# Kernel tuning notes

Measured on AMD Instinct MI355X. Metric: run time of the kernel, lower is better.

The kernel has to match this reference:

```python
import jax, jax.numpy as jnp
import numpy as np

N, E = 50000, 800000
IN, HID, HEADS, EDIM, OUT = 128, 32, 4, 16, 1
W = HID * HEADS  # 128, encoder width


def _glorot(key, shape):
    fan_in = shape[0]
    return jax.random.normal(key, shape, dtype=jnp.float32) / np.sqrt(fan_in)


def setup_inputs() -> dict:
    key = jax.random.key(0)
    ks = jax.random.split(key, 24)
    inp = {
        "x": jax.random.normal(ks[0], (N, IN), dtype=jnp.float32),
        "edge_index": jax.random.randint(ks[1], (2, E), 0, N, dtype=jnp.int64),
        "edge_attr": jax.random.normal(ks[2], (E, EDIM), dtype=jnp.float32),
        # layer 0 (in_channels -> heads*hidden)
        "Wl0": _glorot(ks[3], (IN, W)), "bl0": jnp.zeros((W,), jnp.float32),
        "Wr0": _glorot(ks[4], (IN, W)), "br0": jnp.zeros((W,), jnp.float32),
        "We0": _glorot(ks[5], (EDIM, W)),
        "att0": _glorot(ks[6], (HEADS, HID)),
        "b0": jnp.zeros((W,), jnp.float32),
        # layer 1 (heads*hidden -> heads*hidden)
        "Wl1": _glorot(ks[7], (W, W)), "bl1": jnp.zeros((W,), jnp.float32),
        "Wr1": _glorot(ks[8], (W, W)), "br1": jnp.zeros((W,), jnp.float32),
        "We1": _glorot(ks[9], (EDIM, W)),
        "att1": _glorot(ks[10], (HEADS, HID)),
        "b1": jnp.zeros((W,), jnp.float32),
        # classifier
        "Wc": _glorot(ks[11], (W, OUT)), "bc": jnp.zeros((OUT,), jnp.float32),
    }
    return inp


def _gatv2_layer(x, src, dst, ea, Wl, bl, Wr, br, We, att, b, n_nodes):
    # GATv2Conv (PyG defaults: share_weights=False, negative_slope=0.2, concat=True)
    H, C = att.shape
    xl = (x @ Wl + bl).reshape(n_nodes, H, C)   # source-side transform
    xr = (x @ Wr + br).reshape(n_nodes, H, C)   # target-side transform
    eh = (ea @ We).reshape(-1, H, C)            # edge feature transform (no bias)
    m = xl[src] + xr[dst] + eh                  # [E', H, C] per-edge message pre-activation
    e = jnp.einsum('ehc,hc->eh', jax.nn.leaky_relu(m, 0.2), att)  # [E', H]
    # segment softmax over incoming edges of each dst node (self-loops ensure no empty segment)
    emax = jax.ops.segment_max(e, dst, num_segments=n_nodes)
    ex = jnp.exp(e - emax[dst])
    denom = jax.ops.segment_sum(ex, dst, num_segments=n_nodes)
    alpha = ex / (denom[dst] + 1e-16)
    out = jax.ops.segment_sum(alpha[..., None] * xl[src], dst, num_segments=n_nodes)
    return out.reshape(n_nodes, H * C) + b


def reference(x, edge_index, edge_attr,
              Wl0, bl0, Wr0, br0, We0, att0, b0,
              Wl1, bl1, Wr1, br1, We1, att1, b1,
              Wc, bc):
    n = x.shape[0]
    src, dst = edge_index[0], edge_index[1]
    # add_self_loops with fill_value='mean': self-loop edge_attr = mean of incoming edge_attr per node
    cnt = jax.ops.segment_sum(jnp.ones((src.shape[0],), x.dtype), dst, num_segments=n)
    loop_attr = jax.ops.segment_sum(edge_attr, dst, num_segments=n) / jnp.maximum(cnt, 1.0)[:, None]
    loop = jnp.arange(n, dtype=src.dtype)
    src_a = jnp.concatenate([src, loop])
    dst_a = jnp.concatenate([dst, loop])
    ea_a = jnp.concatenate([edge_attr, loop_attr], axis=0)

    h = jax.nn.gelu(_gatv2_layer(x, src_a, dst_a, ea_a, Wl0, bl0, Wr0, br0, We0, att0, b0, n), approximate=False)
    h = jax.nn.gelu(_gatv2_layer(h, src_a, dst_a, ea_a, Wl1, bl1, Wr1, br1, We1, att1, b1, n), approximate=False)
    logits = h @ Wc + bc  # [N, 1]  (dropout inactive in eval mode)
    return logits.squeeze(-1)
```

## Files before the change

kernel.cpp:

```cpp
#include <hip/hip_runtime.h>
#include <math.h>


static inline size_t align256(size_t x) { return (x + 255) & ~size_t(255); }

__device__ __forceinline__ int clampi(int v, int lo, int hi) {
  return v < lo ? lo : (v > hi ? hi : v);
}

__global__ void k_loop_accum(const int* __restrict__ ei, const float* __restrict__ ea,
                             float* __restrict__ lsum, int* __restrict__ cnt, int E, int n) {
  int i = blockIdx.x * blockDim.x + threadIdx.x;
  if (i >= E * 16) return;
  int e = i >> 4, d = i & 15;
  int dst = clampi(ei[E + e], 0, n - 1);
  atomicAdd(&lsum[dst * 16 + d], ea[i]);
  if (d == 0) atomicAdd(&cnt[dst], 1);
}

__global__ void k_loop_final(float* __restrict__ lsum, const int* __restrict__ cnt, int n) {
  int i = blockIdx.x * blockDim.x + threadIdx.x;
  if (i >= n * 16) return;
  int node = i >> 4;
  int c = cnt[node];
  lsum[i] = lsum[i] / (float)(c > 1 ? c : 1);
}

__global__ void k_scan(const int* __restrict__ cnt, int* __restrict__ row_ptr, int n) {
  const int T = 512;
  __shared__ int wsum[8], wbase[8];
  int tid = threadIdx.x;
  int chunk = (n + T - 1) / T;
  int lo = tid * chunk; if (lo > n) lo = n;
  int hi = lo + chunk;  if (hi > n) hi = n;
  int s = 0;
  for (int i = lo; i < hi; ++i) s += cnt[i] + 1;
  int lane = tid & 63, w = tid >> 6;
  int incl = s;
  #pragma unroll
  for (int d = 1; d < 64; d <<= 1) {
    int v = __shfl_up(incl, d, 64);
    if (lane >= d) incl += v;
  }
  if (lane == 63) wsum[w] = incl;
  __syncthreads();
  if (tid == 0) {
    int a = 0;
    for (int i = 0; i < 8; ++i) { wbase[i] = a; a += wsum[i]; }
  }
  __syncthreads();
  int run = wbase[w] + (incl - s);
  if (tid == 0) row_ptr[0] = 0;
  for (int i = lo; i < hi; ++i) { run += cnt[i] + 1; row_ptr[i + 1] = run; }
}

__global__ void k_scatter(const int* __restrict__ ei, int* __restrict__ cursor,
                          int* __restrict__ col_src, int* __restrict__ col_eid, int E, int n) {
  int i = blockIdx.x * blockDim.x + threadIdx.x;
  if (i < E) {
    int src = clampi(ei[i], 0, n - 1);
    int dst = clampi(ei[E + i], 0, n - 1);
    int pos = atomicAdd(&cursor[dst], 1);
    col_src[pos] = src;
    col_eid[pos] = i;
  } else if (i < E + n) {
    int node = i - E;
    int pos = atomicAdd(&cursor[node], 1);
    col_src[pos] = node;
    col_eid[pos] = E + node;
  }
}

__launch_bounds__(256)
__global__ void k_transform(const float* __restrict__ in, const float* __restrict__ Wl,
                            const float* __restrict__ bl, const float* __restrict__ Wr,
                            const float* __restrict__ br, float* __restrict__ xl,
                            float* __restrict__ xr, int n) {
  __shared__ float As[16][128];
  int tid = threadIdx.x;
  int row0 = blockIdx.x * 16;
  int rows = n - row0; if (rows > 16) rows = 16;
  const float4* in4 = (const float4*)(in + (size_t)row0 * 128);
  float4* As4 = (float4*)As;
  for (int i = tid; i < rows * 32; i += 256) As4[i] = in4[i];
  __syncthreads();
  int c = tid;
  const float* B = (c < 128) ? Wl : Wr;
  int cc = c & 127;
  float bias = (c < 128) ? bl[cc] : br[cc];
  float acc[16];
  #pragma unroll
  for (int i = 0; i < 16; ++i) acc[i] = bias;
  for (int k = 0; k < 128; k += 4) {
    float b0 = B[(k + 0) * 128 + cc], b1 = B[(k + 1) * 128 + cc];
    float b2 = B[(k + 2) * 128 + cc], b3 = B[(k + 3) * 128 + cc];
    #pragma unroll
    for (int r = 0; r < 16; ++r) {
      float4 a = *(const float4*)&As[r][k];
      acc[r] += a.x * b0 + a.y * b1 + a.z * b2 + a.w * b3;
    }
  }
  float* op = (c < 128) ? xl : xr;
  for (int r = 0; r < rows; ++r) op[(size_t)(row0 + r) * 128 + cc] = acc[r];
}

__launch_bounds__(256)
__global__ void k_aggregate(const float* __restrict__ xl, const float* __restrict__ xr,
                            const int* __restrict__ row_ptr, const int* __restrict__ col_src,
                            const int* __restrict__ col_eid, const float* __restrict__ ea,
                            const float* __restrict__ loop_attr, const float* __restrict__ We,
                            const float* __restrict__ att, const float* __restrict__ bvec,
                            float* __restrict__ out, int n, int E) {
  int wv = threadIdx.x >> 6, lane = threadIdx.x & 63;
  int node = blockIdx.x * 4 + wv;
  if (node >= n) return;
  int c0 = lane * 2, c1 = lane * 2 + 1;
  float we0[16], we1[16];
  #pragma unroll
  for (int d = 0; d < 16; ++d) {
    we0[d] = We[d * 128 + c0];
    we1[d] = We[d * 128 + c1];
  }
  float att0 = att[c0], att1 = att[c1];
  float2 xrv = ((const float2*)(xr + (size_t)node * 128))[lane];
  float mx = -INFINITY, den = 0.f, acc0 = 0.f, acc1 = 0.f;
  int beg = row_ptr[node], end = row_ptr[node + 1];
  #pragma unroll 4
  for (int i = beg; i < end; ++i) {
    int src = col_src[i];
    int eid = col_eid[i];
    const float4* eap = (eid < E) ? (const float4*)(ea + (size_t)eid * 16)
                                  : (const float4*)(loop_attr + (size_t)(eid - E) * 16);
    float2 xlv = ((const float2*)(xl + (size_t)src * 128))[lane];
    float eh0 = 0.f, eh1 = 0.f;
    #pragma unroll
    for (int q = 0; q < 4; ++q) {
      float4 v = eap[q];
      eh0 += v.x * we0[q * 4 + 0] + v.y * we0[q * 4 + 1] + v.z * we0[q * 4 + 2] + v.w * we0[q * 4 + 3];
      eh1 += v.x * we1[q * 4 + 0] + v.y * we1[q * 4 + 1] + v.z * we1[q * 4 + 2] + v.w * we1[q * 4 + 3];
    }
    float m0 = xlv.x + xrv.x + eh0;
    float m1 = xlv.y + xrv.y + eh1;
    float l0 = m0 > 0.f ? m0 : 0.2f * m0;
    float l1 = m1 > 0.f ? m1 : 0.2f * m1;
    float p = l0 * att0 + l1 * att1;
    p += __shfl_xor(p, 1);
    p += __shfl_xor(p, 2);
    p += __shfl_xor(p, 4);
    p += __shfl_xor(p, 8);
    float nm = fmaxf(mx, p);
    float sc = expf(mx - nm);
    float w  = expf(p - nm);
    den  = den  * sc + w;
    acc0 = acc0 * sc + w * xlv.x;
    acc1 = acc1 * sc + w * xlv.y;
    mx = nm;
  }
  float inv = 1.f / (den + 1e-16f);
  float2 bv = ((const float2*)bvec)[lane];
  float o0 = acc0 * inv + bv.x;
  float o1 = acc1 * inv + bv.y;
  o0 = 0.5f * o0 * (1.f + erff(o0 * 0.70710678118654752f));
  o1 = 0.5f * o1 * (1.f + erff(o1 * 0.70710678118654752f));
  ((float2*)(out + (size_t)node * 128))[lane] = make_float2(o0, o1);
}

__global__ void k_classifier(const float* __restrict__ h, const float* __restrict__ Wc,
                             const float* __restrict__ bc, float* __restrict__ out, int n) {
  int node = blockIdx.x * blockDim.x + threadIdx.x;
  if (node >= n) return;
  const float4* hp = (const float4*)(h + (size_t)node * 128);
  const float4* wp = (const float4*)Wc;
  float acc = 0.f;
  #pragma unroll
  for (int k = 0; k < 32; ++k) {
    float4 a = hp[k];
    float4 w = wp[k];
    acc += a.x * w.x + a.y * w.y + a.z * w.z + a.w * w.w;
  }
  out[node] = acc + bc[0];
}

extern "C" void kernel_launch(void* const* d_in, const int* in_sizes, int n_in,
                              void* d_out, int out_size, void* d_ws, size_t ws_size,
                              hipStream_t stream) {
  const float* x    = (const float*)d_in[0];
  const int*   ei   = (const int*)d_in[1];
  const float* ea   = (const float*)d_in[2];
  const float* Wl0  = (const float*)d_in[3];
  const float* bl0  = (const float*)d_in[4];
  const float* Wr0  = (const float*)d_in[5];
  const float* br0  = (const float*)d_in[6];
  const float* We0  = (const float*)d_in[7];
  const float* att0 = (const float*)d_in[8];
  const float* b0   = (const float*)d_in[9];
  const float* Wl1  = (const float*)d_in[10];
  const float* bl1  = (const float*)d_in[11];
  const float* Wr1  = (const float*)d_in[12];
  const float* br1  = (const float*)d_in[13];
  const float* We1  = (const float*)d_in[14];
  const float* att1 = (const float*)d_in[15];
  const float* b1   = (const float*)d_in[16];
  const float* Wc   = (const float*)d_in[17];
  const float* bc   = (const float*)d_in[18];
  float* out = (float*)d_out;

  int n  = in_sizes[0] / 128;
  int E  = in_sizes[1] / 2;
  int Ep = E + n;

  char* ws = (char*)d_ws;
  size_t off = 0;
  auto alloc = [&](size_t bytes) { size_t o = off; off = align256(off + bytes); return o; };
  int*   cnt     = (int*)  (ws + alloc((size_t)n * 4));
  float* lsum    = (float*)(ws + alloc((size_t)n * 16 * 4));
  int*   row_ptr = (int*)  (ws + alloc((size_t)(n + 1) * 4));
  int*   cursor  = (int*)  (ws + alloc((size_t)n * 4));
  int*   col_src = (int*)  (ws + alloc((size_t)Ep * 4));
  int*   col_eid = (int*)  (ws + alloc((size_t)Ep * 4));
  float* xl      = (float*)(ws + alloc((size_t)n * 128 * 4));
  float* xr      = (float*)(ws + alloc((size_t)n * 128 * 4));
  float* hbuf    = (float*)(ws + alloc((size_t)n * 128 * 4));
  (void)ws_size; (void)n_in; (void)out_size;

  hipMemsetAsync(cnt, 0, (size_t)n * 4, stream);
  hipMemsetAsync(lsum, 0, (size_t)n * 64, stream);
  k_loop_accum<<<(E * 16 + 255) / 256, 256, 0, stream>>>(ei, ea, lsum, cnt, E, n);
  k_loop_final<<<(n * 16 + 255) / 256, 256, 0, stream>>>(lsum, cnt, n);
  k_scan<<<1, 512, 0, stream>>>(cnt, row_ptr, n);
  hipMemcpyAsync(cursor, row_ptr, (size_t)n * 4, hipMemcpyDeviceToDevice, stream);
  k_scatter<<<(Ep + 255) / 256, 256, 0, stream>>>(ei, cursor, col_src, col_eid, E, n);

  k_transform<<<(n + 15) / 16, 256, 0, stream>>>(x, Wl0, bl0, Wr0, br0, xl, xr, n);
  k_aggregate<<<(n + 3) / 4, 256, 0, stream>>>(xl, xr, row_ptr, col_src, col_eid,
                                               ea, lsum, We0, att0, b0, hbuf, n, E);
  k_transform<<<(n + 15) / 16, 256, 0, stream>>>(hbuf, Wl1, bl1, Wr1, br1, xl, xr, n);
  k_aggregate<<<(n + 3) / 4, 256, 0, stream>>>(xl, xr, row_ptr, col_src, col_eid,
                                               ea, lsum, We1, att1, b1, hbuf, n, E);
  k_classifier<<<(n + 255) / 256, 256, 0, stream>>>(hbuf, Wc, bc, out, n);
}
```

Before: 905.9 us.

## Compute self-loop mean via CSR gather and dual-chain edge aggregation

Replaces the per-element atomic accumulation of self-loop edge attributes with a degree histogram plus a CSR-based gather that computes each node's mean without float atomics. The column arrays are packed into one int2 buffer. The aggregate loop now processes two edges per iteration into two independent online-softmax chains, merged at the end, and uses readfirstlane to keep indices scalar. It also switches to fast __expf and a branchless leaky ReLU. The cost is an extra pass over the CSR in the loop-mean kernel, slightly different float rounding, and more registers in the aggregate kernel.

```diff
diff --git a/kernel.cpp b/kernel.cpp
--- a/kernel.cpp
+++ b/kernel.cpp
@@ -8,27 +8,16 @@
   return v < lo ? lo : (v > hi ? hi : v);
 }
 
-__global__ void k_loop_accum(const int* __restrict__ ei, const float* __restrict__ ea,
-                             float* __restrict__ lsum, int* __restrict__ cnt, int E, int n) {
+__global__ void k_hist(const int* __restrict__ ei, int* __restrict__ cnt, int E, int n) {
   int i = blockIdx.x * blockDim.x + threadIdx.x;
-  if (i >= E * 16) return;
-  int e = i >> 4, d = i & 15;
-  int dst = clampi(ei[E + e], 0, n - 1);
-  atomicAdd(&lsum[dst * 16 + d], ea[i]);
-  if (d == 0) atomicAdd(&cnt[dst], 1);
-}
-
-__global__ void k_loop_final(float* __restrict__ lsum, const int* __restrict__ cnt, int n) {
-  int i = blockIdx.x * blockDim.x + threadIdx.x;
-  if (i >= n * 16) return;
-  int node = i >> 4;
-  int c = cnt[node];
-  lsum[i] = lsum[i] / (float)(c > 1 ? c : 1);
+  if (i >= E) return;
+  int dst = clampi(ei[E + i], 0, n - 1);
+  atomicAdd(&cnt[dst], 1);
 }
 
 __global__ void k_scan(const int* __restrict__ cnt, int* __restrict__ row_ptr, int n) {
-  const int T = 512;
-  __shared__ int wsum[8], wbase[8];
+  const int T = 1024;
+  __shared__ int wsum[16], wbase[16];
   int tid = threadIdx.x;
   int chunk = (n + T - 1) / T;
   int lo = tid * chunk; if (lo > n) lo = n;
@@ -46,7 +35,7 @@
   __syncthreads();
   if (tid == 0) {
     int a = 0;
-    for (int i = 0; i < 8; ++i) { wbase[i] = a; a += wsum[i]; }
+    for (int i = 0; i < 16; ++i) { wbase[i] = a; a += wsum[i]; }
   }
   __syncthreads();
   int run = wbase[w] + (incl - s);
@@ -55,20 +44,34 @@
 }
 
 __global__ void k_scatter(const int* __restrict__ ei, int* __restrict__ cursor,
-                          int* __restrict__ col_src, int* __restrict__ col_eid, int E, int n) {
+                          int2* __restrict__ col, int E, int n) {
   int i = blockIdx.x * blockDim.x + threadIdx.x;
   if (i < E) {
     int src = clampi(ei[i], 0, n - 1);
     int dst = clampi(ei[E + i], 0, n - 1);
     int pos = atomicAdd(&cursor[dst], 1);
-    col_src[pos] = src;
-    col_eid[pos] = i;
+    col[pos] = make_int2(src, i);
   } else if (i < E + n) {
     int node = i - E;
     int pos = atomicAdd(&cursor[node], 1);
-    col_src[pos] = node;
-    col_eid[pos] = E + node;
-  }
+    col[pos] = make_int2(node, E + node);
+  }
+}
+
+__global__ void k_loop_mean(const int* __restrict__ row_ptr, const int2* __restrict__ col,
+                            const float* __restrict__ ea, float* __restrict__ lsum,
+                            int n, int E) {
+  int t = blockIdx.x * blockDim.x + threadIdx.x;
+  if (t >= n * 16) return;
+  int node = t >> 4, d = t & 15;
+  int beg = row_ptr[node], end = row_ptr[node + 1];
+  float s = 0.f;
+  int c = 0;
+  for (int i = beg; i < end; ++i) {
+    int2 se = col[i];
+    if (se.y < E) { s += ea[(size_t)se.y * 16 + d]; ++c; }
+  }
+  lsum[t] = s / (float)(c > 0 ? c : 1);
 }
 
 __launch_bounds__(256)
@@ -104,13 +107,48 @@
   for (int r = 0; r < rows; ++r) op[(size_t)(row0 + r) * 128 + cc] = acc[r];
 }
 
+#define EDGE_STEP(SRC, EID, MX, DEN, A0, A1)                                     \
+  do {                                                                           \
+    const float* ep = ((EID) < E) ? (ea + (size_t)(EID) * 16)                    \
+                                  : (loop_attr + (size_t)((EID) - E) * 16);      \
+    float2 xlv = *(const float2*)(xl + (size_t)(SRC) * 128 + lane * 2);          \
+    float4 v0 = ((const float4*)ep)[0];                                          \
+    float4 v1 = ((const float4*)ep)[1];                                          \
+    float4 v2 = ((const float4*)ep)[2];                                          \
+    float4 v3 = ((const float4*)ep)[3];                                          \
+    float eh0 = v0.x * we0[0] + v0.y * we0[1] + v0.z * we0[2] + v0.w * we0[3];   \
+    float eh1 = v0.x * we1[0] + v0.y * we1[1] + v0.z * we1[2] + v0.w * we1[3];   \
+    eh0 += v1.x * we0[4] + v1.y * we0[5] + v1.z * we0[6] + v1.w * we0[7];        \
+    eh1 += v1.x * we1[4] + v1.y * we1[5] + v1.z * we1[6] + v1.w * we1[7];        \
+    eh0 += v2.x * we0[8] + v2.y * we0[9] + v2.z * we0[10] + v2.w * we0[11];      \
+    eh1 += v2.x * we1[8] + v2.y * we1[9] + v2.z * we1[10] + v2.w * we1[11];      \
+    eh0 += v3.x * we0[12] + v3.y * we0[13] + v3.z * we0[14] + v3.w * we0[15];    \
+    eh1 += v3.x * we1[12] + v3.y * we1[13] + v3.z * we1[14] + v3.w * we1[15];    \
+    float m0 = xlv.x + xrv.x + eh0;                                              \
+    float m1 = xlv.y + xrv.y + eh1;                                              \
+    float l0 = fmaxf(m0, 0.2f * m0);                        \
+    float l1 = fmaxf(m1, 0.2f * m1);                                             \
+    float p = l0 * att0 + l1 * att1;                                             \
+    p += __shfl_xor(p, 1);                                                       \
+    p += __shfl_xor(p, 2);                                                       \
+    p += __shfl_xor(p, 4);                                                       \
+    p += __shfl_xor(p, 8);                                                       \
+    float nm = fmaxf(MX, p);                                                     \
+    float sc = __expf(MX - nm);                                                  \
+    float w  = __expf(p - nm);                                                   \
+    DEN = DEN * sc + w;                                                          \
+    A0  = A0 * sc + w * xlv.x;                                                   \
+    A1  = A1 * sc + w * xlv.y;                                                   \
+    MX  = nm;                                                                    \
+  } while (0)
+
 __launch_bounds__(256)
 __global__ void k_aggregate(const float* __restrict__ xl, const float* __restrict__ xr,
-                            const int* __restrict__ row_ptr, const int* __restrict__ col_src,
-                            const int* __restrict__ col_eid, const float* __restrict__ ea,
-                            const float* __restrict__ loop_attr, const float* __restrict__ We,
-                            const float* __restrict__ att, const float* __restrict__ bvec,
-                            float* __restrict__ out, int n, int E) {
+                            const int* __restrict__ row_ptr, const int2* __restrict__ col,
+                            const float* __restrict__ ea, const float* __restrict__ loop_attr,
+                            const float* __restrict__ We, const float* __restrict__ att,
+                            const float* __restrict__ bvec, float* __restrict__ out,
+                            int n, int E) {
   int wv = threadIdx.x >> 6, lane = threadIdx.x & 63;
   int node = blockIdx.x * 4 + wv;
   if (node >= n) return;
@@ -122,47 +160,41 @@
     we1[d] = We[d * 128 + c1];
   }
   float att0 = att[c0], att1 = att[c1];
-  float2 xrv = ((const float2*)(xr + (size_t)node * 128))[lane];
-  float mx = -INFINITY, den = 0.f, acc0 = 0.f, acc1 = 0.f;
-  int beg = row_ptr[node], end = row_ptr[node + 1];
-  #pragma unroll 4
-  for (int i = beg; i < end; ++i) {
-    int src = col_src[i];
-    int eid = col_eid[i];
-    const float4* eap = (eid < E) ? (const float4*)(ea + (size_t)eid * 16)
-                                  : (const float4*)(loop_attr + (size_t)(eid - E) * 16);
-    float2 xlv = ((const float2*)(xl + (size_t)src * 128))[lane];
-    float eh0 = 0.f, eh1 = 0.f;
-    #pragma unroll
-    for (int q = 0; q < 4; ++q) {
-      float4 v = eap[q];
-      eh0 += v.x * we0[q * 4 + 0] + v.y * we0[q * 4 + 1] + v.z * we0[q * 4 + 2] + v.w * we0[q * 4 + 3];
-      eh1 += v.x * we1[q * 4 + 0] + v.y * we1[q * 4 + 1] + v.z * we1[q * 4 + 2] + v.w * we1[q * 4 + 3];
-    }
-    float m0 = xlv.x + xrv.x + eh0;
-    float m1 = xlv.y + xrv.y + eh1;
-    float l0 = m0 > 0.f ? m0 : 0.2f * m0;
-    float l1 = m1 > 0.f ? m1 : 0.2f * m1;
-    float p = l0 * att0 + l1 * att1;
-    p += __shfl_xor(p, 1);
-    p += __shfl_xor(p, 2);
-    p += __shfl_xor(p, 4);
-    p += __shfl_xor(p, 8);
-    float nm = fmaxf(mx, p);
-    float sc = expf(mx - nm);
-    float w  = expf(p - nm);
-    den  = den  * sc + w;
-    acc0 = acc0 * sc + w * xlv.x;
-    acc1 = acc1 * sc + w * xlv.y;
-    mx = nm;
-  }
+  float2 xrv = *(const float2*)(xr + (size_t)node * 128 + lane * 2);
+  int beg = __builtin_amdgcn_readfirstlane(row_ptr[node]);
+  int end = __builtin_amdgcn_readfirstlane(row_ptr[node + 1]);
+  float mA = -INFINITY, dA = 0.f, a0A = 0.f, a1A = 0.f;
+  float mB = -INFINITY, dB = 0.f, a0B = 0.f, a1B = 0.f;
+  int i = beg;
+  #pragma unroll 2
+  for (; i + 1 < end; i += 2) {
+    int2 sa = col[i];
+    int2 sb = col[i + 1];
+    int srcA = __builtin_amdgcn_readfirstlane(sa.x);
+    int eidA = __builtin_amdgcn_readfirstlane(sa.y);
+    int srcB = __builtin_amdgcn_readfirstlane(sb.x);
+    int eidB = __builtin_amdgcn_readfirstlane(sb.y);
+    EDGE_STEP(srcA, eidA, mA, dA, a0A, a1A);
+    EDGE_STEP(srcB, eidB, mB, dB, a0B, a1B);
+  }
+  if (i < end) {
+    int2 sa = col[i];
+    int srcA = __builtin_amdgcn_readfirstlane(sa.x);
+    int eidA = __builtin_amdgcn_readfirstlane(sa.y);
+    EDGE_STEP(srcA, eidA, mA, dA, a0A, a1A);
+  }
+  float nm = fmaxf(mA, mB);
+  float eA = __expf(mA - nm), eB = __expf(mB - nm);
+  float den  = dA * eA + dB * eB;
+  float acc0 = a0A * eA + a0B * eB;
+  float acc1 = a1A * eA + a1B * eB;
   float inv = 1.f / (den + 1e-16f);
   float2 bv = ((const float2*)bvec)[lane];
   float o0 = acc0 * inv + bv.x;
   float o1 = acc1 * inv + bv.y;
   o0 = 0.5f * o0 * (1.f + erff(o0 * 0.70710678118654752f));
   o1 = 0.5f * o1 * (1.f + erff(o1 * 0.70710678118654752f));
-  ((float2*)(out + (size_t)node * 128))[lane] = make_float2(o0, o1);
+  *(float2*)(out + (size_t)node * 128 + lane * 2) = make_float2(o0, o1);
 }
 
 __global__ void k_classifier(const float* __restrict__ h, const float* __restrict__ Wc,
@@ -216,26 +248,24 @@
   float* lsum    = (float*)(ws + alloc((size_t)n * 16 * 4));
   int*   row_ptr = (int*)  (ws + alloc((size_t)(n + 1) * 4));
   int*   cursor  = (int*)  (ws + alloc((size_t)n * 4));
-  int*   col_src = (int*)  (ws + alloc((size_t)Ep * 4));
-  int*   col_eid = (int*)  (ws + alloc((size_t)Ep * 4));
+  int2*  col     = (int2*) (ws + alloc((size_t)Ep * 8));
   float* xl      = (float*)(ws + alloc((size_t)n * 128 * 4));
   float* xr      = (float*)(ws + alloc((size_t)n * 128 * 4));
   float* hbuf    = (float*)(ws + alloc((size_t)n * 128 * 4));
   (void)ws_size; (void)n_in; (void)out_size;
 
   hipMemsetAsync(cnt, 0, (size_t)n * 4, stream);
-  hipMemsetAsync(lsum, 0, (size_t)n * 64, stream);
-  k_loop_accum<<<(E * 16 + 255) / 256, 256, 0, stream>>>(ei, ea, lsum, cnt, E, n);
-  k_loop_final<<<(n * 16 + 255) / 256, 256, 0, stream>>>(lsum, cnt, n);
-  k_scan<<<1, 512, 0, stream>>>(cnt, row_ptr, n);
+  k_hist<<<(E + 255) / 256, 256, 0, stream>>>(ei, cnt, E, n);
+  k_scan<<<1, 1024, 0, stream>>>(cnt, row_ptr, n);
   hipMemcpyAsync(cursor, row_ptr, (size_t)n * 4, hipMemcpyDeviceToDevice, stream);
-  k_scatter<<<(Ep + 255) / 256, 256, 0, stream>>>(ei, cursor, col_src, col_eid, E, n);
+  k_scatter<<<(Ep + 255) / 256, 256, 0, stream>>>(ei, cursor, col, E, n);
+  k_loop_mean<<<(n * 16 + 255) / 256, 256, 0, stream>>>(row_ptr, col, ea, lsum, n, E);
 
   k_transform<<<(n + 15) / 16, 256, 0, stream>>>(x, Wl0, bl0, Wr0, br0, xl, xr, n);
-  k_aggregate<<<(n + 3) / 4, 256, 0, stream>>>(xl, xr, row_ptr, col_src, col_eid,
-                                               ea, lsum, We0, att0, b0, hbuf, n, E);
+  k_aggregate<<<(n + 3) / 4, 256, 0, stream>>>(xl, xr, row_ptr, col, ea, lsum,
+                                               We0, att0, b0, hbuf, n, E);
   k_transform<<<(n + 15) / 16, 256, 0, stream>>>(hbuf, Wl1, bl1, Wr1, br1, xl, xr, n);
-  k_aggregate<<<(n + 3) / 4, 256, 0, stream>>>(xl, xr, row_ptr, col_src, col_eid,
-                                               ea, lsum, We1, att1, b1, hbuf, n, E);
+  k_aggregate<<<(n + 3) / 4, 256, 0, stream>>>(xl, xr, row_ptr, col, ea, lsum,
+                                               We1, att1, b1, hbuf, n, E);
   k_classifier<<<(n + 255) / 256, 256, 0, stream>>>(hbuf, Wc, bc, out, n);
 }
```

After: 821.0 us. -9.4%, faster.
